# Performance work log

Measured on AMD Instinct MI355X. Metric: run time of the kernel, lower is better.

Reference implementation:

```python
import jax, jax.numpy as jnp
import numpy as np
from jax import lax

NPOINT = 1024   # num_points (FPS centroids)
RADIUS = 0.2    # ball-query radius
K = 32          # samples per ball
FILTERS = [64, 64, 128]


def setup_inputs() -> dict:
    key = jax.random.key(0)
    ks = jax.random.split(key, 10)
    B, N, C = 16, 4096, 64
    xyz = jax.random.uniform(ks[0], (B, N, 3), dtype=jnp.float32)   # unit-cube cloud
    points = jax.random.normal(ks[1], (B, N, C), dtype=jnp.float32)
    inp = {"xyz": xyz, "points": points}
    cin = C + 3  # use_xyz=True concatenates relative xyz
    for i, f in enumerate(FILTERS):
        scale = np.sqrt(2.0 / (cin + f)).astype(np.float32)  # glorot_normal
        inp[f"w{i}"] = jax.random.normal(ks[2 + i], (cin, f), dtype=jnp.float32) * scale
        inp[f"b{i}"] = jnp.zeros((f,), dtype=jnp.float32)
        cin = f
    return inp


def farthest_point_sample(xyz, npoint):
    # Serial greedy FPS. xyz: [B,N,3] -> idx [B,npoint] int32
    B, N, _ = xyz.shape

    def body(carry, _):
        dist, far = carry                                   # [B,N], [B]
        centroid = jnp.take_along_axis(xyz, far[:, None, None], axis=1)  # [B,1,3]
        d = jnp.sum((xyz - centroid) ** 2, axis=-1)         # [B,N]
        dist = jnp.minimum(dist, d)
        nxt = jnp.argmax(dist, axis=-1).astype(jnp.int32)
        return (dist, nxt), far

    init = (jnp.full((B, N), 1e10, xyz.dtype), jnp.zeros((B,), jnp.int32))
    _, idxs = lax.scan(body, init, None, length=npoint)
    return idxs.T  # [B,npoint]


def query_ball(radius, nsample, xyz, new_xyz):
    # First-nsample-in-order points within radius; pad with first hit (CUDA semantics).
    B, N, _ = xyz.shape
    d2 = jnp.sum((new_xyz[:, :, None, :] - xyz[:, None, :, :]) ** 2, axis=-1)  # [B,S,N]
    mask = d2 <= radius * radius
    order = jnp.where(mask, jnp.arange(N, dtype=jnp.int32)[None, None, :], N)
    idx_sorted = jnp.sort(order, axis=-1)[..., :nsample]    # first K valid indices
    first = idx_sorted[..., :1]
    first = jnp.where(first < N, first, 0)                  # empty-ball fallback
    return jnp.where(idx_sorted < N, idx_sorted, first)     # [B,S,K]


def reference(xyz, points, w0, b0, w1, b1, w2, b2):
    B, N, _ = xyz.shape
    fps_idx = farthest_point_sample(xyz, NPOINT)                    # [B,S]
    new_xyz = jnp.take_along_axis(xyz, fps_idx[:, :, None], axis=1)  # [B,S,3]
    idx = query_ball(RADIUS, K, xyz, new_xyz)                        # [B,S,K]

    bix = jnp.arange(B)[:, None, None]
    grouped_xyz = xyz[bix, idx] - new_xyz[:, :, None, :]             # [B,S,K,3] recentered
    grouped_pts = points[bix, idx]                                   # [B,S,K,C]
    g = jnp.concatenate([grouped_pts, grouped_xyz], axis=-1)         # [B,S,K,C+3]

    for w, b in ((w0, b0), (w1, b1), (w2, b2)):                      # shared 1x1-conv MLP
        g = jax.nn.relu(jnp.einsum('bskc,cf->bskf', g, w) + b)
    new_points = jnp.max(g, axis=2)                                  # max-pool over ball
    return new_xyz, new_points
```

## Files before the change

### kernel.cpp

```cpp
#include <hip/hip_runtime.h>
#include <stdint.h>

#define BB 16
#define NN 4096
#define CC 64
#define NPOINT 1024
#define KK 32
#define F1 64
#define F2 64
#define F3 128

#define FPS_T 512
#define PPT (NN / FPS_T)

#if defined(__has_builtin)
#if __has_builtin(__builtin_amdgcn_update_dpp)
#define HAS_DPP 1
#endif
#endif

#ifdef HAS_DPP
template <int CTRL>
__device__ __forceinline__ unsigned long long dpp_move64(unsigned long long k) {
    int lo = __builtin_amdgcn_update_dpp(0, (int)(unsigned)k,         CTRL, 0xF, 0xF, false);
    int hi = __builtin_amdgcn_update_dpp(0, (int)(unsigned)(k >> 32), CTRL, 0xF, 0xF, false);
    return ((unsigned long long)(unsigned)hi << 32) | (unsigned)lo;
}
__device__ __forceinline__ unsigned long long wave_max_key(unsigned long long key) {
    unsigned long long o;
    o = dpp_move64<0x111>(key); if (o > key) key = o;
    o = dpp_move64<0x112>(key); if (o > key) key = o;
    o = dpp_move64<0x114>(key); if (o > key) key = o;
    o = dpp_move64<0x118>(key); if (o > key) key = o;
    o = dpp_move64<0x142>(key); if (o > key) key = o;
    o = dpp_move64<0x143>(key); if (o > key) key = o;
    return key;
}
#else
__device__ __forceinline__ unsigned long long wave_max_key(unsigned long long key) {
#pragma unroll
    for (int off = 32; off > 0; off >>= 1) {
        unsigned long long o = __shfl_xor(key, off, 64);
        if (o > key) key = o;
    }
    return key;
}
#endif

#define SMEM_BYTES 49664

__global__ __launch_bounds__(512)
void fused_kernel(const float* __restrict__ xyz,
                  const float* __restrict__ points,
                  const float* __restrict__ w0, const float* __restrict__ b0,
                  const float* __restrict__ w1, const float* __restrict__ b1,
                  const float* __restrict__ w2, const float* __restrict__ b2,
                  float* __restrict__ out_xyz,
                  float* __restrict__ out_points,
                  int* __restrict__ ctr) {
    __shared__ __align__(16) char smem[SMEM_BYTES];
    const int tid = threadIdx.x;

    if (blockIdx.x < BB) {
        asm volatile("s_setprio 3");
        float* xs = (float*)smem;
        float* ys = xs + NN;
        float* zs = ys + NN;
        unsigned long long (*wred)[FPS_T / 64] =
            (unsigned long long (*)[FPS_T / 64])(smem + 49152);
        float* cbuf = (float*)(smem + 49280);

        const int b = blockIdx.x;
        const int lane = tid & 63, wid = tid >> 6;
        const float* __restrict__ xb = xyz + (size_t)b * (NN * 3);

        float px[PPT], py[PPT], pz[PPT], dist[PPT];
#pragma unroll
        for (int t = 0; t < PPT; ++t) {
            int p = tid + t * FPS_T;
            px[t] = xb[p * 3 + 0];
            py[t] = xb[p * 3 + 1];
            pz[t] = xb[p * 3 + 2];
            xs[p] = px[t]; ys[p] = py[t]; zs[p] = pz[t];
            dist[t] = 1e10f;
        }
        __syncthreads();

        float cx = xs[0], cy = ys[0], cz = zs[0];
        float* xo = out_xyz + (size_t)b * NPOINT * 3;

        for (int i = 0; i < NPOINT; ++i) {
            if (tid == 0) {
                cbuf[(i & 7) * 3 + 0] = cx;
                cbuf[(i & 7) * 3 + 1] = cy;
                cbuf[(i & 7) * 3 + 2] = cz;
            }
            float bd = -1.0f; int bp = 0;
#pragma unroll
            for (int t = 0; t < PPT; ++t) {
                float dx = __fsub_rn(px[t], cx);
                float dy = __fsub_rn(py[t], cy);
                float dz = __fsub_rn(pz[t], cz);
                float d  = __fadd_rn(__fadd_rn(__fmul_rn(dx, dx), __fmul_rn(dy, dy)),
                                     __fmul_rn(dz, dz));
                float nd = fminf(dist[t], d);
                dist[t] = nd;
                if (nd > bd) { bd = nd; bp = tid + t * FPS_T; }
            }
            unsigned long long key = (((unsigned long long)__float_as_uint(bd)) << 32)
                                   | (unsigned int)(NN - 1 - bp);
            key = wave_max_key(key);
            if (lane == 63) wred[i & 1][wid] = key;
            __syncthreads();

            unsigned long long best = wred[i & 1][0];
#pragma unroll
            for (int w = 1; w < FPS_T / 64; ++w) {
                unsigned long long o = wred[i & 1][w];
                if (o > best) best = o;
            }
            int bi = (NN - 1) - (int)(best & 0xffffffffu);

            if (tid == 0 && (i & 7) == 7) {
                const float4* src = (const float4*)cbuf;
                float4* dst = (float4*)(xo + (size_t)(i - 7) * 3);
                dst[0] = src[0]; dst[1] = src[1]; dst[2] = src[2];
                dst[3] = src[3]; dst[4] = src[4]; dst[5] = src[5];
                __hip_atomic_store(&ctr[b * 16], i + 1,
                                   __ATOMIC_RELEASE, __HIP_MEMORY_SCOPE_AGENT);
            }
            cx = xs[bi]; cy = ys[bi]; cz = zs[bi];
        }
    } else {
        float (*gbuf)[68] = (float (*)[68])smem;
        float (*hbuf)[F1] = (float (*)[F1])(smem + 8704);
        float (*pmax)[F3] = (float (*)[F3])(smem + 16896);
        unsigned long long* cmask = (unsigned long long*)(smem + 20992);
        int* nbr = (int*)(smem + 21504);

        const int gi = blockIdx.x - BB;
        const int s = gi >> 4;
        const int b = gi & 15;
        const int g = b * NPOINT + s;
        const int f = tid & 63;
        const int wid = tid >> 6;

        if (tid == 0) {
            while (__hip_atomic_load(&ctr[b * 16], __ATOMIC_RELAXED,
                                     __HIP_MEMORY_SCOPE_AGENT) < s + 1)
                __builtin_amdgcn_s_sleep(2);
            (void)__hip_atomic_load(&ctr[b * 16], __ATOMIC_ACQUIRE,
                                    __HIP_MEMORY_SCOPE_AGENT);
        }
        __syncthreads();

        unsigned int ux = __hip_atomic_load((unsigned int*)&out_xyz[(size_t)g * 3 + 0],
                                            __ATOMIC_RELAXED, __HIP_MEMORY_SCOPE_AGENT);
        unsigned int uy = __hip_atomic_load((unsigned int*)&out_xyz[(size_t)g * 3 + 1],
                                            __ATOMIC_RELAXED, __HIP_MEMORY_SCOPE_AGENT);
        unsigned int uz = __hip_atomic_load((unsigned int*)&out_xyz[(size_t)g * 3 + 2],
                                            __ATOMIC_RELAXED, __HIP_MEMORY_SCOPE_AGENT);
        const float cx = __uint_as_float(ux);
        const float cy = __uint_as_float(uy);
        const float cz = __uint_as_float(uz);

        {
            const float* __restrict__ xb = xyz + (size_t)b * (NN * 3);
#pragma unroll
            for (int j = 0; j < 8; ++j) {
                int chunk = wid * 8 + j;
                int p = chunk * 64 + f;
                float x = xb[p * 3 + 0];
                float y = xb[p * 3 + 1];
                float z = xb[p * 3 + 2];
                float dx = __fsub_rn(cx, x);
                float dy = __fsub_rn(cy, y);
                float dz = __fsub_rn(cz, z);
                float d2 = __fadd_rn(__fadd_rn(__fmul_rn(dx, dx), __fmul_rn(dy, dy)),
                                     __fmul_rn(dz, dz));
                unsigned long long m = __ballot(d2 <= 0.04f);
                if (f == 0) cmask[chunk] = m;
            }
        }
        __syncthreads();

        if (tid < 64) {
            unsigned long long m = cmask[tid];
            int cnt = (int)__popcll(m);
            int v = cnt;
#pragma unroll
            for (int off = 1; off < 64; off <<= 1) {
                int u = __shfl_up(v, off, 64);
                if (tid >= off) v += u;
            }
            int excl = v - cnt;
            int total = __shfl(v, 63, 64);
            unsigned long long mm = m;
            int r = excl;
            while (mm && r < KK) {
                int bpos = __ffsll(mm) - 1;
                mm &= mm - 1;
                nbr[r++] = tid * 64 + bpos;
            }
            if (total < KK) {
                unsigned long long nz = __ballot(cnt > 0);
                int fchunk = __ffsll(nz) - 1;
                unsigned long long fm = cmask[fchunk];
                int first = fchunk * 64 + __ffsll(fm) - 1;
                if (tid >= total && tid < KK) nbr[tid] = first;
            }
        }
        __syncthreads();

        {
            const float* __restrict__ pb = points + (size_t)b * NN * CC;
#pragma unroll
            for (int m = 0; m < 4; ++m) {
                int k = wid + 8 * m;
                int idx = nbr[k] & (NN - 1);
                gbuf[k][f] = pb[(size_t)idx * CC + f];
            }
            if (tid < 96) {
                int k = tid & 31, q = tid >> 5;
                int idx = nbr[k] & (NN - 1);
                float v = xyz[((size_t)b * NN + idx) * 3 + q];
                float cq = (q == 0) ? cx : ((q == 1) ? cy : cz);
                gbuf[k][CC + q] = __fsub_rn(v, cq);
            }
        }
        __syncthreads();

        float acc[4];

#pragma unroll
        for (int m = 0; m < 4; ++m) acc[m] = 0.0f;
#pragma unroll 4
        for (int c4 = 0; c4 < 64; c4 += 4) {
            float wv0 = w0[(c4 + 0) * F1 + f];
            float wv1 = w0[(c4 + 1) * F1 + f];
            float wv2 = w0[(c4 + 2) * F1 + f];
            float wv3 = w0[(c4 + 3) * F1 + f];
#pragma unroll
            for (int m = 0; m < 4; ++m) {
                float4 gv = *(const float4*)&gbuf[wid + 8 * m][c4];
                acc[m] = fmaf(gv.x, wv0, acc[m]);
                acc[m] = fmaf(gv.y, wv1, acc[m]);
                acc[m] = fmaf(gv.z, wv2, acc[m]);
                acc[m] = fmaf(gv.w, wv3, acc[m]);
            }
        }
        {
            float wv0 = w0[64 * F1 + f];
            float wv1 = w0[65 * F1 + f];
            float wv2 = w0[66 * F1 + f];
#pragma unroll
            for (int m = 0; m < 4; ++m) {
                int k = wid + 8 * m;
                acc[m] = fmaf(gbuf[k][64], wv0, acc[m]);
                acc[m] = fmaf(gbuf[k][65], wv1, acc[m]);
                acc[m] = fmaf(gbuf[k][66], wv2, acc[m]);
            }
        }
        {
            float bb = b0[f];
#pragma unroll
            for (int m = 0; m < 4; ++m)
                hbuf[wid + 8 * m][f] = fmaxf(acc[m] + bb, 0.0f);
        }
        __syncthreads();

#pragma unroll
        for (int m = 0; m < 4; ++m) acc[m] = 0.0f;
#pragma unroll 4
        for (int c4 = 0; c4 < 64; c4 += 4) {
            float wv0 = w1[(c4 + 0) * F2 + f];
            float wv1 = w1[(c4 + 1) * F2 + f];
            float wv2 = w1[(c4 + 2) * F2 + f];
            float wv3 = w1[(c4 + 3) * F2 + f];
#pragma unroll
            for (int m = 0; m < 4; ++m) {
                float4 gv = *(const float4*)&hbuf[wid + 8 * m][c4];
                acc[m] = fmaf(gv.x, wv0, acc[m]);
                acc[m] = fmaf(gv.y, wv1, acc[m]);
                acc[m] = fmaf(gv.z, wv2, acc[m]);
                acc[m] = fmaf(gv.w, wv3, acc[m]);
            }
        }
        {
            float bb = b1[f];
#pragma unroll
            for (int m = 0; m < 4; ++m)
                gbuf[wid + 8 * m][f] = fmaxf(acc[m] + bb, 0.0f);
        }
        __syncthreads();

        float a0[4], a1[4];
#pragma unroll
        for (int m = 0; m < 4; ++m) { a0[m] = 0.0f; a1[m] = 0.0f; }
#pragma unroll 2
        for (int c4 = 0; c4 < 64; c4 += 4) {
            float w00 = w2[(c4 + 0) * F3 + f], w10 = w2[(c4 + 0) * F3 + f + 64];
            float w01 = w2[(c4 + 1) * F3 + f], w11 = w2[(c4 + 1) * F3 + f + 64];
            float w02 = w2[(c4 + 2) * F3 + f], w12 = w2[(c4 + 2) * F3 + f + 64];
            float w03 = w2[(c4 + 3) * F3 + f], w13 = w2[(c4 + 3) * F3 + f + 64];
#pragma unroll
            for (int m = 0; m < 4; ++m) {
                float4 gv = *(const float4*)&gbuf[wid + 8 * m][c4];
                a0[m] = fmaf(gv.x, w00, a0[m]);  a1[m] = fmaf(gv.x, w10, a1[m]);
                a0[m] = fmaf(gv.y, w01, a0[m]);  a1[m] = fmaf(gv.y, w11, a1[m]);
                a0[m] = fmaf(gv.z, w02, a0[m]);  a1[m] = fmaf(gv.z, w12, a1[m]);
                a0[m] = fmaf(gv.w, w03, a0[m]);  a1[m] = fmaf(gv.w, w13, a1[m]);
            }
        }
        {
            float pm0 = -1e30f, pm1 = -1e30f;
#pragma unroll
            for (int m = 0; m < 4; ++m) {
                pm0 = fmaxf(pm0, a0[m]);
                pm1 = fmaxf(pm1, a1[m]);
            }
            pmax[wid][f] = pm0;
            pmax[wid][f + 64] = pm1;
        }
        __syncthreads();
        if (tid < F3) {
            float v = pmax[0][tid];
#pragma unroll
            for (int w = 1; w < 8; ++w) v = fmaxf(v, pmax[w][tid]);
            v = fmaxf(v + b2[tid], 0.0f);
            out_points[(size_t)g * F3 + tid] = v;
        }
    }
}

extern "C" void kernel_launch(void* const* d_in, const int* in_sizes, int n_in,
                              void* d_out, int out_size, void* d_ws, size_t ws_size,
                              hipStream_t stream) {
    const float* xyz    = (const float*)d_in[0];
    const float* points = (const float*)d_in[1];
    const float* w0 = (const float*)d_in[2];
    const float* b0 = (const float*)d_in[3];
    const float* w1 = (const float*)d_in[4];
    const float* b1 = (const float*)d_in[5];
    const float* w2 = (const float*)d_in[6];
    const float* b2 = (const float*)d_in[7];

    float* out_xyz    = (float*)d_out;
    float* out_points = out_xyz + (size_t)BB * NPOINT * 3;
    int*   ctr        = (int*)d_ws;

    fused_kernel<<<BB + BB * NPOINT, 512, 0, stream>>>(
        xyz, points, w0, b0, w1, b1, w2, b2, out_xyz, out_points, ctr);
}
```

Measured before the change: 815.0 us.

## Pack FPS and MLP math into float2 ops and stage weights in LDS

The FPS loop now keeps coordinates and distances as float2 vectors so the compiler can emit packed FP32 ops. The argmax is found with a max tree followed by an equality scan, instead of a compare inside the loop. In the MLP blocks, the weights for each layer are staged into shared memory (w2 in two column halves), and the dot products use packed FMA with split even/odd accumulators. The aim is fewer VALU instructions on the serial FPS critical path and fewer global weight loads. The cost is extra barriers, weight copies into LDS, and accumulation-order changes in the MLP.

```diff
diff --git a/kernel.cpp b/kernel.cpp
--- a/kernel.cpp
+++ b/kernel.cpp
@@ -12,6 +12,8 @@
 
 #define FPS_T 512
 #define PPT (NN / FPS_T)
+
+typedef float v2f __attribute__((ext_vector_type(2)));
 
 #if defined(__has_builtin)
 #if __has_builtin(__builtin_amdgcn_update_dpp)
@@ -74,15 +76,19 @@
         const int lane = tid & 63, wid = tid >> 6;
         const float* __restrict__ xb = xyz + (size_t)b * (NN * 3);
 
-        float px[PPT], py[PPT], pz[PPT], dist[PPT];
-#pragma unroll
-        for (int t = 0; t < PPT; ++t) {
-            int p = tid + t * FPS_T;
-            px[t] = xb[p * 3 + 0];
-            py[t] = xb[p * 3 + 1];
-            pz[t] = xb[p * 3 + 2];
-            xs[p] = px[t]; ys[p] = py[t]; zs[p] = pz[t];
-            dist[t] = 1e10f;
+        v2f px2[4], py2[4], pz2[4], dd[4];
+#pragma unroll
+        for (int j = 0; j < 4; ++j) {
+#pragma unroll
+            for (int h = 0; h < 2; ++h) {
+                int p = tid + (2 * j + h) * FPS_T;
+                float x = xb[p * 3 + 0];
+                float y = xb[p * 3 + 1];
+                float z = xb[p * 3 + 2];
+                px2[j][h] = x; py2[j][h] = y; pz2[j][h] = z;
+                xs[p] = x; ys[p] = y; zs[p] = z;
+            }
+            dd[j] = (v2f){1e10f, 1e10f};
         }
         __syncthreads();
 
@@ -95,17 +101,27 @@
                 cbuf[(i & 7) * 3 + 1] = cy;
                 cbuf[(i & 7) * 3 + 2] = cz;
             }
-            float bd = -1.0f; int bp = 0;
-#pragma unroll
-            for (int t = 0; t < PPT; ++t) {
-                float dx = __fsub_rn(px[t], cx);
-                float dy = __fsub_rn(py[t], cy);
-                float dz = __fsub_rn(pz[t], cz);
-                float d  = __fadd_rn(__fadd_rn(__fmul_rn(dx, dx), __fmul_rn(dy, dy)),
-                                     __fmul_rn(dz, dz));
-                float nd = fminf(dist[t], d);
-                dist[t] = nd;
-                if (nd > bd) { bd = nd; bp = tid + t * FPS_T; }
+            {
+#pragma clang fp contract(off)
+                v2f c2x = (v2f){cx, cx}, c2y = (v2f){cy, cy}, c2z = (v2f){cz, cz};
+#pragma unroll
+                for (int j = 0; j < 4; ++j) {
+                    v2f dx = px2[j] - c2x;
+                    v2f dy = py2[j] - c2y;
+                    v2f dz = pz2[j] - c2z;
+                    v2f ss = (dx * dx + dy * dy) + dz * dz;
+                    dd[j] = __builtin_elementwise_min(dd[j], ss);
+                }
+            }
+            v2f m01 = __builtin_elementwise_max(dd[0], dd[1]);
+            v2f m23 = __builtin_elementwise_max(dd[2], dd[3]);
+            v2f mm  = __builtin_elementwise_max(m01, m23);
+            float bd = fmaxf(mm.x, mm.y);
+            int bp = 0;
+#pragma unroll
+            for (int j = 3; j >= 0; --j) {
+                if (dd[j].y == bd) bp = tid + (2 * j + 1) * FPS_T;
+                if (dd[j].x == bd) bp = tid + (2 * j + 0) * FPS_T;
             }
             unsigned long long key = (((unsigned long long)__float_as_uint(bd)) << 32)
                                    | (unsigned int)(NN - 1 - bp);
@@ -137,6 +153,8 @@
         float (*pmax)[F3] = (float (*)[F3])(smem + 16896);
         unsigned long long* cmask = (unsigned long long*)(smem + 20992);
         int* nbr = (int*)(smem + 21504);
+        float* wbuf = (float*)(smem + 21632);
+        float4* wbuf4 = (float4*)wbuf;
 
         const int gi = blockIdx.x - BB;
         const int s = gi >> 4;
@@ -144,6 +162,12 @@
         const int g = b * NPOINT + s;
         const int f = tid & 63;
         const int wid = tid >> 6;
+
+        {
+            const float4* src = (const float4*)w0;
+#pragma unroll
+            for (int i = tid; i < 1072; i += 512) wbuf4[i] = src[i];
+        }
 
         if (tid == 0) {
             while (__hip_atomic_load(&ctr[b * 16], __ATOMIC_RELAXED,
@@ -230,99 +254,99 @@
         }
         __syncthreads();
 
-        float acc[4];
-
-#pragma unroll
-        for (int m = 0; m < 4; ++m) acc[m] = 0.0f;
+        v2f acc2[4];
+
+#pragma unroll
+        for (int m = 0; m < 4; ++m) acc2[m] = (v2f){0.0f, 0.0f};
 #pragma unroll 4
         for (int c4 = 0; c4 < 64; c4 += 4) {
-            float wv0 = w0[(c4 + 0) * F1 + f];
-            float wv1 = w0[(c4 + 1) * F1 + f];
-            float wv2 = w0[(c4 + 2) * F1 + f];
-            float wv3 = w0[(c4 + 3) * F1 + f];
+            v2f w01 = (v2f){wbuf[(c4 + 0) * F1 + f], wbuf[(c4 + 1) * F1 + f]};
+            v2f w23 = (v2f){wbuf[(c4 + 2) * F1 + f], wbuf[(c4 + 3) * F1 + f]};
 #pragma unroll
             for (int m = 0; m < 4; ++m) {
                 float4 gv = *(const float4*)&gbuf[wid + 8 * m][c4];
-                acc[m] = fmaf(gv.x, wv0, acc[m]);
-                acc[m] = fmaf(gv.y, wv1, acc[m]);
-                acc[m] = fmaf(gv.z, wv2, acc[m]);
-                acc[m] = fmaf(gv.w, wv3, acc[m]);
-            }
-        }
-        {
-            float wv0 = w0[64 * F1 + f];
-            float wv1 = w0[65 * F1 + f];
-            float wv2 = w0[66 * F1 + f];
+                acc2[m] = __builtin_elementwise_fma((v2f){gv.x, gv.y}, w01, acc2[m]);
+                acc2[m] = __builtin_elementwise_fma((v2f){gv.z, gv.w}, w23, acc2[m]);
+            }
+        }
+        {
+            float wv0 = wbuf[64 * F1 + f];
+            float wv1 = wbuf[65 * F1 + f];
+            float wv2 = wbuf[66 * F1 + f];
+            float bb = b0[f];
 #pragma unroll
             for (int m = 0; m < 4; ++m) {
                 int k = wid + 8 * m;
-                acc[m] = fmaf(gbuf[k][64], wv0, acc[m]);
-                acc[m] = fmaf(gbuf[k][65], wv1, acc[m]);
-                acc[m] = fmaf(gbuf[k][66], wv2, acc[m]);
-            }
-        }
-        {
-            float bb = b0[f];
-#pragma unroll
-            for (int m = 0; m < 4; ++m)
-                hbuf[wid + 8 * m][f] = fmaxf(acc[m] + bb, 0.0f);
-        }
-        __syncthreads();
-
-#pragma unroll
-        for (int m = 0; m < 4; ++m) acc[m] = 0.0f;
+                float a = acc2[m].x + acc2[m].y;
+                a = fmaf(gbuf[k][64], wv0, a);
+                a = fmaf(gbuf[k][65], wv1, a);
+                a = fmaf(gbuf[k][66], wv2, a);
+                hbuf[k][f] = fmaxf(a + bb, 0.0f);
+            }
+        }
+        __syncthreads();
+
+        {
+            const float4* src = (const float4*)w1;
+#pragma unroll
+            for (int i = tid; i < 1024; i += 512) wbuf4[i] = src[i];
+        }
+        __syncthreads();
+
+#pragma unroll
+        for (int m = 0; m < 4; ++m) acc2[m] = (v2f){0.0f, 0.0f};
 #pragma unroll 4
         for (int c4 = 0; c4 < 64; c4 += 4) {
-            float wv0 = w1[(c4 + 0) * F2 + f];
-            float wv1 = w1[(c4 + 1) * F2 + f];
-            float wv2 = w1[(c4 + 2) * F2 + f];
-            float wv3 = w1[(c4 + 3) * F2 + f];
+            v2f w01 = (v2f){wbuf[(c4 + 0) * F2 + f], wbuf[(c4 + 1) * F2 + f]};
+            v2f w23 = (v2f){wbuf[(c4 + 2) * F2 + f], wbuf[(c4 + 3) * F2 + f]};
 #pragma unroll
             for (int m = 0; m < 4; ++m) {
                 float4 gv = *(const float4*)&hbuf[wid + 8 * m][c4];
-                acc[m] = fmaf(gv.x, wv0, acc[m]);
-                acc[m] = fmaf(gv.y, wv1, acc[m]);
-                acc[m] = fmaf(gv.z, wv2, acc[m]);
-                acc[m] = fmaf(gv.w, wv3, acc[m]);
+                acc2[m] = __builtin_elementwise_fma((v2f){gv.x, gv.y}, w01, acc2[m]);
+                acc2[m] = __builtin_elementwise_fma((v2f){gv.z, gv.w}, w23, acc2[m]);
             }
         }
         {
             float bb = b1[f];
 #pragma unroll
             for (int m = 0; m < 4; ++m)
-                gbuf[wid + 8 * m][f] = fmaxf(acc[m] + bb, 0.0f);
-        }
-        __syncthreads();
-
-        float a0[4], a1[4];
-#pragma unroll
-        for (int m = 0; m < 4; ++m) { a0[m] = 0.0f; a1[m] = 0.0f; }
-#pragma unroll 2
-        for (int c4 = 0; c4 < 64; c4 += 4) {
-            float w00 = w2[(c4 + 0) * F3 + f], w10 = w2[(c4 + 0) * F3 + f + 64];
-            float w01 = w2[(c4 + 1) * F3 + f], w11 = w2[(c4 + 1) * F3 + f + 64];
-            float w02 = w2[(c4 + 2) * F3 + f], w12 = w2[(c4 + 2) * F3 + f + 64];
-            float w03 = w2[(c4 + 3) * F3 + f], w13 = w2[(c4 + 3) * F3 + f + 64];
-#pragma unroll
-            for (int m = 0; m < 4; ++m) {
-                float4 gv = *(const float4*)&gbuf[wid + 8 * m][c4];
-                a0[m] = fmaf(gv.x, w00, a0[m]);  a1[m] = fmaf(gv.x, w10, a1[m]);
-                a0[m] = fmaf(gv.y, w01, a0[m]);  a1[m] = fmaf(gv.y, w11, a1[m]);
-                a0[m] = fmaf(gv.z, w02, a0[m]);  a1[m] = fmaf(gv.z, w12, a1[m]);
-                a0[m] = fmaf(gv.w, w03, a0[m]);  a1[m] = fmaf(gv.w, w13, a1[m]);
-            }
-        }
-        {
-            float pm0 = -1e30f, pm1 = -1e30f;
-#pragma unroll
-            for (int m = 0; m < 4; ++m) {
-                pm0 = fmaxf(pm0, a0[m]);
-                pm1 = fmaxf(pm1, a1[m]);
-            }
-            pmax[wid][f] = pm0;
-            pmax[wid][f + 64] = pm1;
-        }
-        __syncthreads();
+                gbuf[wid + 8 * m][f] = fmaxf(acc2[m].x + acc2[m].y + bb, 0.0f);
+        }
+        __syncthreads();
+
+#pragma unroll
+        for (int h = 0; h < 2; ++h) {
+            {
+                const float4* src = (const float4*)w2;
+#pragma unroll
+                for (int i = tid; i < 1024; i += 512) {
+                    int c = i >> 4, col4 = i & 15;
+                    wbuf4[i] = src[c * 32 + 16 * h + col4];
+                }
+            }
+            __syncthreads();
+#pragma unroll
+            for (int m = 0; m < 4; ++m) acc2[m] = (v2f){0.0f, 0.0f};
+#pragma unroll 4
+            for (int c4 = 0; c4 < 64; c4 += 4) {
+                v2f w01 = (v2f){wbuf[(c4 + 0) * 64 + f], wbuf[(c4 + 1) * 64 + f]};
+                v2f w23 = (v2f){wbuf[(c4 + 2) * 64 + f], wbuf[(c4 + 3) * 64 + f]};
+#pragma unroll
+                for (int m = 0; m < 4; ++m) {
+                    float4 gv = *(const float4*)&gbuf[wid + 8 * m][c4];
+                    acc2[m] = __builtin_elementwise_fma((v2f){gv.x, gv.y}, w01, acc2[m]);
+                    acc2[m] = __builtin_elementwise_fma((v2f){gv.z, gv.w}, w23, acc2[m]);
+                }
+            }
+            {
+                float pm = -1e30f;
+#pragma unroll
+                for (int m = 0; m < 4; ++m) pm = fmaxf(pm, acc2[m].x + acc2[m].y);
+                pmax[wid][f + 64 * h] = pm;
+            }
+            __syncthreads();
+        }
+
         if (tid < F3) {
             float v = pmax[0][tid];
 #pragma unroll
```

Result: slower. 836.8 us (+2.7%).
